# Kernel tuning notes

Hardware: AMD Instinct MI355X
Metric: run time of the kernel (lower is better)

## Reference

```python
import jax, jax.numpy as jnp
import numpy as np

N = 50000      # nodes
E = 500000     # edges (before self-loops)
IN = 128       # input feature dim
HID = 64       # hidden per head
HEADS = 8
OUT = 40       # classes
NEG_SLOPE = 0.2  # PyG GATConv default


def setup_inputs() -> dict:
    key = jax.random.key(0)
    ks = jax.random.split(key, 10)
    s = 0.05
    return {
        "x": jax.random.normal(ks[0], (N, IN), jnp.float32),
        "edge_index": jax.random.randint(ks[1], (2, E), 0, N, dtype=jnp.int32),
        "W1": jax.random.normal(ks[2], (IN, HEADS * HID), jnp.float32) * s,
        "a1_src": jax.random.normal(ks[3], (HEADS, HID), jnp.float32) * s,
        "a1_dst": jax.random.normal(ks[4], (HEADS, HID), jnp.float32) * s,
        "b1": jnp.zeros((HEADS * HID,), jnp.float32),
        "W2": jax.random.normal(ks[5], (HEADS * HID, OUT), jnp.float32) * s,
        "a2_src": jax.random.normal(ks[6], (1, OUT), jnp.float32) * s,
        "a2_dst": jax.random.normal(ks[7], (1, OUT), jnp.float32) * s,
        "b2": jnp.zeros((OUT,), jnp.float32),
    }


def gat_layer(x, src, dst, W, a_src, a_dst, b, heads, ch, concat):
    n = x.shape[0]
    h = (x @ W).reshape(n, heads, ch)                    # [N,H,C]
    e_src = jnp.einsum('nhc,hc->nh', h, a_src)           # [N,H]
    e_dst = jnp.einsum('nhc,hc->nh', h, a_dst)
    logits = jax.nn.leaky_relu(e_src[src] + e_dst[dst], NEG_SLOPE)  # [E,H]
    # segment softmax over incoming edges of each dst node
    m = jax.ops.segment_max(logits, dst, num_segments=n)
    p = jnp.exp(logits - m[dst])
    z = jax.ops.segment_sum(p, dst, num_segments=n)
    alpha = p / (z[dst] + 1e-16)                         # [E,H]
    out = jax.ops.segment_sum(h[src] * alpha[:, :, None], dst, num_segments=n)  # [N,H,C]
    out = out.reshape(n, heads * ch) if concat else out.mean(axis=1)
    return out + b


def reference(x, edge_index, W1, a1_src, a1_dst, b1, W2, a2_src, a2_dst, b2):
    loops = jnp.arange(N, dtype=edge_index.dtype)
    src = jnp.concatenate([edge_index[0], loops])        # add self-loops (PyG default)
    dst = jnp.concatenate([edge_index[1], loops])
    h = jax.nn.relu(gat_layer(x, src, dst, W1, a1_src, a1_dst, b1, HEADS, HID, True))
    h = gat_layer(h, src, dst, W2, a2_src, a2_dst, b2, 1, OUT, False)
    return jax.nn.log_softmax(h, axis=1)
```

## Files before the change

### kernel.cpp

```cpp
#include <hip/hip_runtime.h>
#include <math.h>

#define N_NODES 50000
#define E_EDGES 500000
#define E_TOT   550000
#define IN_DIM  128
#define HID     64
#define HEADS   8
#define HC      512
#define OUT_DIM 40
#define NEG_SLOPE 0.2f

__device__ __forceinline__ float leaky(float v){ return v > 0.f ? v : NEG_SLOPE * v; }


__global__ void k_hist(const int* __restrict__ ei, int* __restrict__ counts){
    int i = blockIdx.x * 256 + threadIdx.x;
    if (i < E_EDGES){
        atomicAdd(&counts[ei[E_EDGES + i]], 1);
    } else if (i < E_TOT){
        atomicAdd(&counts[i - E_EDGES], 1);
    }
}

__global__ void k_scanA(const int* __restrict__ counts, int* __restrict__ offsets,
                        int* __restrict__ blockSums){
    __shared__ int sh[1024];
    int b = blockIdx.x, t = threadIdx.x;
    int i = b * 1024 + t;
    int v = (i < N_NODES) ? counts[i] : 0;
    sh[t] = v; __syncthreads();
    for (int off = 1; off < 1024; off <<= 1){
        int add = (t >= off) ? sh[t - off] : 0;
        __syncthreads();
        sh[t] += add;
        __syncthreads();
    }
    if (i < N_NODES) offsets[i + 1] = sh[t];
    if (t == 1023) blockSums[b] = sh[t];
}

__global__ void k_scanB(int* __restrict__ blockSums, int nb){
    if (threadIdx.x == 0 && blockIdx.x == 0){
        int run = 0;
        for (int b = 0; b < nb; b++){ int v = blockSums[b]; blockSums[b] = run; run += v; }
    }
}

__global__ void k_scanC(const int* __restrict__ counts, int* __restrict__ offsets,
                        const int* __restrict__ blockSums, int* __restrict__ cursor){
    int b = blockIdx.x, t = threadIdx.x;
    int i = b * 1024 + t;
    if (i < N_NODES){
        int v = offsets[i + 1] + blockSums[b];
        offsets[i + 1] = v;
        cursor[i] = v - counts[i];
    }
    if (i == 0) offsets[0] = 0;
}

__global__ void k_scatter(const int* __restrict__ ei, int* __restrict__ cursor,
                          int* __restrict__ sortedSrc){
    int i = blockIdx.x * 256 + threadIdx.x;
    if (i < E_EDGES){
        int d = ei[E_EDGES + i];
        int pos = atomicAdd(&cursor[d], 1);
        sortedSrc[pos] = ei[i];
    } else if (i < E_TOT){
        int n = i - E_EDGES;
        int pos = atomicAdd(&cursor[n], 1);
        sortedSrc[pos] = n;
    }
}


__global__ __launch_bounds__(256) void k_gemm1e1(const float* __restrict__ x,
                                                 const float* __restrict__ W1,
                                                 const float* __restrict__ a1s,
                                                 const float* __restrict__ a1d,
                                                 float* __restrict__ h1,
                                                 float* __restrict__ e1s,
                                                 float* __restrict__ e1d){
    __shared__ float xs[16 * IN_DIM];
    const int t = threadIdx.x;
    const int row0 = blockIdx.x * 16;
    const float4* xg = (const float4*)(x + (size_t)row0 * IN_DIM);
    float4* xsv = (float4*)xs;
    xsv[t] = xg[t];
    xsv[t + 256] = xg[t + 256];
    __syncthreads();

    const int ct = t & 127;
    const int rg = t >> 7;
    float4 acc[8];
    #pragma unroll
    for (int r = 0; r < 8; r++) acc[r] = make_float4(0.f, 0.f, 0.f, 0.f);

    const float4* Wv = (const float4*)W1;
    for (int kb = 0; kb < IN_DIM; kb += 4){
        float4 w0 = Wv[(size_t)(kb + 0) * 128 + ct];
        float4 w1 = Wv[(size_t)(kb + 1) * 128 + ct];
        float4 w2 = Wv[(size_t)(kb + 2) * 128 + ct];
        float4 w3 = Wv[(size_t)(kb + 3) * 128 + ct];
        #pragma unroll
        for (int r = 0; r < 8; r++){
            float4 xv = *(const float4*)&xs[(rg * 8 + r) * IN_DIM + kb];
            acc[r].x = fmaf(xv.x, w0.x, acc[r].x); acc[r].y = fmaf(xv.x, w0.y, acc[r].y);
            acc[r].z = fmaf(xv.x, w0.z, acc[r].z); acc[r].w = fmaf(xv.x, w0.w, acc[r].w);
            acc[r].x = fmaf(xv.y, w1.x, acc[r].x); acc[r].y = fmaf(xv.y, w1.y, acc[r].y);
            acc[r].z = fmaf(xv.y, w1.z, acc[r].z); acc[r].w = fmaf(xv.y, w1.w, acc[r].w);
            acc[r].x = fmaf(xv.z, w2.x, acc[r].x); acc[r].y = fmaf(xv.z, w2.y, acc[r].y);
            acc[r].z = fmaf(xv.z, w2.z, acc[r].z); acc[r].w = fmaf(xv.z, w2.w, acc[r].w);
            acc[r].x = fmaf(xv.w, w3.x, acc[r].x); acc[r].y = fmaf(xv.w, w3.y, acc[r].y);
            acc[r].z = fmaf(xv.w, w3.z, acc[r].z); acc[r].w = fmaf(xv.w, w3.w, acc[r].w);
        }
    }

    const float4 as4 = ((const float4*)a1s)[ct];
    const float4 ad4 = ((const float4*)a1d)[ct];
    float4* h1v = (float4*)h1;
    float ps[8], pd[8];
    #pragma unroll
    for (int r = 0; r < 8; r++){
        int row = row0 + rg * 8 + r;
        h1v[(size_t)row * 128 + ct] = acc[r];
        ps[r] = acc[r].x * as4.x + acc[r].y * as4.y + acc[r].z * as4.z + acc[r].w * as4.w;
        pd[r] = acc[r].x * ad4.x + acc[r].y * ad4.y + acc[r].z * ad4.z + acc[r].w * ad4.w;
    }
    #pragma unroll
    for (int off = 1; off < 16; off <<= 1){
        #pragma unroll
        for (int r = 0; r < 8; r++){
            ps[r] += __shfl_xor(ps[r], off, 64);
            pd[r] += __shfl_xor(pd[r], off, 64);
        }
    }
    if ((t & 15) == 0){
        int h = (ct >> 4) & 7;
        #pragma unroll
        for (int r = 0; r < 8; r++){
            int row = row0 + rg * 8 + r;
            e1s[(size_t)row * HEADS + h] = ps[r];
            e1d[(size_t)row * HEADS + h] = pd[r];
        }
    }
}


__global__ __launch_bounds__(256) void k_agg1(const float* __restrict__ h1,
                                              const float* __restrict__ e1s,
                                              const float* __restrict__ e1d,
                                              const int* __restrict__ offsets,
                                              const int* __restrict__ sortedSrc,
                                              const float* __restrict__ b1,
                                              float* __restrict__ hmid){
    __shared__ int   ss[2][64];
    __shared__ float wl[2][64][8];
    __shared__ float zr[8];
    const int d = blockIdx.x;
    const int t = threadIdx.x;
    const int beg = offsets[d], end = offsets[d + 1];
    const int cnt = end - beg;
    const int nch = (cnt + 63) >> 6;
    if (t < 8) zr[t] = 0.f;

    const int jp = t & 3;
    const int el = t >> 2;
    const int hch = t >> 5;
    const float2 ed2 = *(const float2*)&e1d[(size_t)d * HEADS + 2 * jp];
    float2 zacc = make_float2(0.f, 0.f);
    float2 acc  = make_float2(0.f, 0.f);

    {
        int e = beg + el;
        if (e < end){
            int s = sortedSrc[e];
            if (jp == 0) ss[0][el] = s;
            float2 es = *(const float2*)&e1s[(size_t)s * HEADS + 2 * jp];
            float wx = __expf(leaky(es.x + ed2.x));
            float wy = __expf(leaky(es.y + ed2.y));
            *(float2*)&wl[0][el][2 * jp] = make_float2(wx, wy);
            zacc.x += wx; zacc.y += wy;
        }
    }
    __syncthreads();

    for (int c = 0; c < nch; ++c){
        int pb = c & 1;
        if (c + 1 < nch){
            int e = beg + (c + 1) * 64 + el;
            if (e < end){
                int s = sortedSrc[e];
                if (jp == 0) ss[pb ^ 1][el] = s;
                float2 es = *(const float2*)&e1s[(size_t)s * HEADS + 2 * jp];
                float wx = __expf(leaky(es.x + ed2.x));
                float wy = __expf(leaky(es.y + ed2.y));
                *(float2*)&wl[pb ^ 1][el][2 * jp] = make_float2(wx, wy);
                zacc.x += wx; zacc.y += wy;
            }
        }
        int m = cnt - c * 64; if (m > 64) m = 64;
        for (int e = 0; e < m; ++e){
            int s = ss[pb][e];
            float wv = wl[pb][e][hch];
            float2 hv = *(const float2*)&h1[(size_t)s * HC + 2 * t];
            acc.x = fmaf(wv, hv.x, acc.x);
            acc.y = fmaf(wv, hv.y, acc.y);
        }
        __syncthreads();
    }

    atomicAdd(&zr[2 * jp],     zacc.x);
    atomicAdd(&zr[2 * jp + 1], zacc.y);
    __syncthreads();
    float inv = 1.f / (zr[hch] + 1e-16f);
    float2 bv = *(const float2*)&b1[2 * t];
    float ox = fmaxf(fmaf(acc.x, inv, bv.x), 0.f);
    float oy = fmaxf(fmaf(acc.y, inv, bv.y), 0.f);
    *(float2*)&hmid[(size_t)d * HC + 2 * t] = make_float2(ox, oy);
}


__global__ __launch_bounds__(256) void k_gemm2e2(const float* __restrict__ hmid,
                                                 const float* __restrict__ W2,
                                                 const float* __restrict__ a2s,
                                                 const float* __restrict__ a2d,
                                                 float* __restrict__ h2,
                                                 float* __restrict__ e2s,
                                                 float* __restrict__ e2d){
    __shared__ float hs[64][64];
    __shared__ float ws[64 * OUT_DIM];
    const int t = threadIdx.x;
    const int row0 = blockIdx.x * 64;
    const int col = t & 63;
    const int rbase = t >> 6;
    float acc[16];
    #pragma unroll
    for (int i = 0; i < 16; i++) acc[i] = 0.f;

    for (int kb = 0; kb < HC; kb += 64){
        for (int i = t; i < 64 * 64; i += 256){
            int r = i >> 6, k = i & 63;
            int gr = row0 + r;
            hs[r][k] = (gr < N_NODES) ? hmid[(size_t)gr * HC + kb + k] : 0.f;
        }
        for (int i = t; i < 64 * OUT_DIM; i += 256){
            int k = i / OUT_DIM, j = i - k * OUT_DIM;
            ws[i] = W2[(size_t)(kb + k) * OUT_DIM + j];
        }
        __syncthreads();
        if (col < OUT_DIM){
            for (int k = 0; k < 64; k++){
                float w = ws[k * OUT_DIM + col];
                #pragma unroll
                for (int i = 0; i < 16; i++)
                    acc[i] = fmaf(hs[rbase + 4 * i][k], w, acc[i]);
            }
        }
        __syncthreads();
    }

    const float as = (col < OUT_DIM) ? a2s[col] : 0.f;
    const float ad = (col < OUT_DIM) ? a2d[col] : 0.f;
    #pragma unroll
    for (int i = 0; i < 16; i++){
        int r = row0 + rbase + 4 * i;
        bool ok = (col < OUT_DIM) && (r < N_NODES);
        float v = ok ? acc[i] : 0.f;
        if (ok) h2[(size_t)r * OUT_DIM + col] = v;
        float pvs = v * as, pvd = v * ad;
        #pragma unroll
        for (int off = 32; off > 0; off >>= 1){
            pvs += __shfl_xor(pvs, off, 64);
            pvd += __shfl_xor(pvd, off, 64);
        }
        if (col == 0 && r < N_NODES){ e2s[r] = pvs; e2d[r] = pvd; }
    }
}

__global__ __launch_bounds__(64) void k_agg2(const float* __restrict__ h2,
                                             const float* __restrict__ e2s,
                                             const float* __restrict__ e2d,
                                             const int* __restrict__ offsets,
                                             const int* __restrict__ sortedSrc,
                                             const float* __restrict__ b2,
                                             float* __restrict__ out){
    int d = blockIdx.x;
    int lane = threadIdx.x;
    int beg = offsets[d], end = offsets[d + 1];
    float ed = e2d[d];
    float acc = 0.f, z = 0.f;
    for (int e = beg; e < end; e++){
        int s = sortedSrc[e];
        float w = __expf(leaky(e2s[s] + ed));
        z += w;
        if (lane < OUT_DIM) acc = fmaf(w, h2[(size_t)s * OUT_DIM + lane], acc);
    }
    float o = acc / (z + 1e-16f) + ((lane < OUT_DIM) ? b2[lane] : 0.f);
    float ov = (lane < OUT_DIM) ? o : -INFINITY;
    float vmax = ov;
    #pragma unroll
    for (int off = 32; off > 0; off >>= 1) vmax = fmaxf(vmax, __shfl_xor(vmax, off, 64));
    float se = (lane < OUT_DIM) ? __expf(o - vmax) : 0.f;
    #pragma unroll
    for (int off = 32; off > 0; off >>= 1) se += __shfl_xor(se, off, 64);
    if (lane < OUT_DIM) out[(size_t)d * OUT_DIM + lane] = o - vmax - __logf(se);
}


extern "C" void kernel_launch(void* const* d_in, const int* in_sizes, int n_in,
                              void* d_out, int out_size, void* d_ws, size_t ws_size,
                              hipStream_t stream){
    const float* x   = (const float*)d_in[0];
    const int*   ei  = (const int*)  d_in[1];
    const float* W1  = (const float*)d_in[2];
    const float* a1s = (const float*)d_in[3];
    const float* a1d = (const float*)d_in[4];
    const float* b1  = (const float*)d_in[5];
    const float* W2  = (const float*)d_in[6];
    const float* a2s = (const float*)d_in[7];
    const float* a2d = (const float*)d_in[8];
    const float* b2  = (const float*)d_in[9];
    float* out = (float*)d_out;

    char* ws = (char*)d_ws;
    size_t off = 0;
    auto alloc = [&](size_t bytes) -> char* {
        off = (off + 255) & ~(size_t)255;
        char* p = ws + off;
        off += bytes;
        return p;
    };

    float* h1      = (float*)alloc((size_t)N_NODES * HC * 4);
    float* hmid    = (float*)alloc((size_t)N_NODES * HC * 4);
    float* h2      = (float*)alloc((size_t)N_NODES * OUT_DIM * 4);
    float* e1s     = (float*)alloc((size_t)N_NODES * HEADS * 4);
    float* e1d     = (float*)alloc((size_t)N_NODES * HEADS * 4);
    float* e2s     = (float*)alloc((size_t)N_NODES * 4);
    float* e2d     = (float*)alloc((size_t)N_NODES * 4);
    int* counts    = (int*)alloc((size_t)N_NODES * 4);
    int* offsets   = (int*)alloc((size_t)(N_NODES + 1) * 4);
    int* cursor    = (int*)alloc((size_t)N_NODES * 4);
    int* blockSums = (int*)alloc(64 * 4);
    int* sortedSrc = (int*)alloc((size_t)E_TOT * 4);

    const int nb = (N_NODES + 1023) / 1024;

    hipMemsetAsync(counts, 0, (size_t)N_NODES * 4, stream);
    k_hist   <<<(E_TOT + 255) / 256, 256, 0, stream>>>(ei, counts);
    k_scanA  <<<nb, 1024, 0, stream>>>(counts, offsets, blockSums);
    k_scanB  <<<1, 64, 0, stream>>>(blockSums, nb);
    k_scanC  <<<nb, 1024, 0, stream>>>(counts, offsets, blockSums, cursor);
    k_scatter<<<(E_TOT + 255) / 256, 256, 0, stream>>>(ei, cursor, sortedSrc);

    k_gemm1e1<<<N_NODES / 16, 256, 0, stream>>>(x, W1, a1s, a1d, h1, e1s, e1d);
    k_agg1   <<<N_NODES, 256, 0, stream>>>(h1, e1s, e1d, offsets, sortedSrc, b1, hmid);

    k_gemm2e2<<<(N_NODES + 63) / 64, 256, 0, stream>>>(hmid, W2, a2s, a2d, h2, e2s, e2d);
    k_agg2   <<<N_NODES, 64, 0, stream>>>(h2, e2s, e2d, offsets, sortedSrc, b2, out);
}
```

Before: 663.0 us.

## Map one wavefront per destination node in both aggregation kernels with register prefetch

Both aggregation kernels now assign one 64-lane wavefront to each destination node and pack four nodes per 256-thread block. Layer 1 drops the shared-memory double buffer, the block barriers and the shared atomics: each lane owns 8 channels of one head and computes that head's edge weight itself. Both kernels now load the next edge's source index and features into registers one step ahead. This removes block-level sync overhead and the idle threads in blocks that handle few edges. The cost is that the exp is recomputed in each lane, and each wave walks its edge list serially with less memory-level parallelism per node.

```diff
diff --git a/kernel.cpp b/kernel.cpp
--- a/kernel.cpp
+++ b/kernel.cpp
@@ -154,70 +154,58 @@
                                               const int* __restrict__ sortedSrc,
                                               const float* __restrict__ b1,
                                               float* __restrict__ hmid){
-    __shared__ int   ss[2][64];
-    __shared__ float wl[2][64][8];
-    __shared__ float zr[8];
-    const int d = blockIdx.x;
-    const int t = threadIdx.x;
+    const int lane = threadIdx.x & 63;
+    const int d = blockIdx.x * 4 + (threadIdx.x >> 6);
+    if (d >= N_NODES) return;
     const int beg = offsets[d], end = offsets[d + 1];
     const int cnt = end - beg;
-    const int nch = (cnt + 63) >> 6;
-    if (t < 8) zr[t] = 0.f;
-
-    const int jp = t & 3;
-    const int el = t >> 2;
-    const int hch = t >> 5;
-    const float2 ed2 = *(const float2*)&e1d[(size_t)d * HEADS + 2 * jp];
-    float2 zacc = make_float2(0.f, 0.f);
-    float2 acc  = make_float2(0.f, 0.f);
-
+    const int h = lane >> 3;
+    const int c0 = lane * 8;
+    const float ed = e1d[(size_t)d * HEADS + h];
+
+    float4 acc0 = make_float4(0.f,0.f,0.f,0.f), acc1 = make_float4(0.f,0.f,0.f,0.f);
+    float z = 0.f;
+
+    int s1 = 0, s2 = 0;
+    float eA = 0.f; float4 hA0, hA1;
     {
-        int e = beg + el;
-        if (e < end){
-            int s = sortedSrc[e];
-            if (jp == 0) ss[0][el] = s;
-            float2 es = *(const float2*)&e1s[(size_t)s * HEADS + 2 * jp];
-            float wx = __expf(leaky(es.x + ed2.x));
-            float wy = __expf(leaky(es.y + ed2.y));
-            *(float2*)&wl[0][el][2 * jp] = make_float2(wx, wy);
-            zacc.x += wx; zacc.y += wy;
-        }
-    }
-    __syncthreads();
-
-    for (int c = 0; c < nch; ++c){
-        int pb = c & 1;
-        if (c + 1 < nch){
-            int e = beg + (c + 1) * 64 + el;
-            if (e < end){
-                int s = sortedSrc[e];
-                if (jp == 0) ss[pb ^ 1][el] = s;
-                float2 es = *(const float2*)&e1s[(size_t)s * HEADS + 2 * jp];
-                float wx = __expf(leaky(es.x + ed2.x));
-                float wy = __expf(leaky(es.y + ed2.y));
-                *(float2*)&wl[pb ^ 1][el][2 * jp] = make_float2(wx, wy);
-                zacc.x += wx; zacc.y += wy;
-            }
-        }
-        int m = cnt - c * 64; if (m > 64) m = 64;
-        for (int e = 0; e < m; ++e){
-            int s = ss[pb][e];
-            float wv = wl[pb][e][hch];
-            float2 hv = *(const float2*)&h1[(size_t)s * HC + 2 * t];
-            acc.x = fmaf(wv, hv.x, acc.x);
-            acc.y = fmaf(wv, hv.y, acc.y);
-        }
-        __syncthreads();
-    }
-
-    atomicAdd(&zr[2 * jp],     zacc.x);
-    atomicAdd(&zr[2 * jp + 1], zacc.y);
-    __syncthreads();
-    float inv = 1.f / (zr[hch] + 1e-16f);
-    float2 bv = *(const float2*)&b1[2 * t];
-    float ox = fmaxf(fmaf(acc.x, inv, bv.x), 0.f);
-    float oy = fmaxf(fmaf(acc.y, inv, bv.y), 0.f);
-    *(float2*)&hmid[(size_t)d * HC + 2 * t] = make_float2(ox, oy);
+        int s0 = sortedSrc[beg];
+        eA = e1s[(size_t)s0 * HEADS + h];
+        const float4* hp = (const float4*)(h1 + (size_t)s0 * HC + c0);
+        hA0 = hp[0]; hA1 = hp[1];
+        if (cnt > 1) s1 = sortedSrc[beg + 1];
+    }
+    for (int e = 0; e < cnt; ++e){
+        if (e + 2 < cnt) s2 = sortedSrc[beg + e + 2];
+        float eB = 0.f; float4 hB0, hB1;
+        if (e + 1 < cnt){
+            eB = e1s[(size_t)s1 * HEADS + h];
+            const float4* hp = (const float4*)(h1 + (size_t)s1 * HC + c0);
+            hB0 = hp[0]; hB1 = hp[1];
+        }
+        float w = __expf(leaky(eA + ed));
+        z += w;
+        acc0.x = fmaf(w, hA0.x, acc0.x); acc0.y = fmaf(w, hA0.y, acc0.y);
+        acc0.z = fmaf(w, hA0.z, acc0.z); acc0.w = fmaf(w, hA0.w, acc0.w);
+        acc1.x = fmaf(w, hA1.x, acc1.x); acc1.y = fmaf(w, hA1.y, acc1.y);
+        acc1.z = fmaf(w, hA1.z, acc1.z); acc1.w = fmaf(w, hA1.w, acc1.w);
+        eA = eB; hA0 = hB0; hA1 = hB1; s1 = s2;
+    }
+
+    const float inv = 1.f / (z + 1e-16f);
+    const float4 bv0 = ((const float4*)b1)[lane * 2];
+    const float4 bv1 = ((const float4*)b1)[lane * 2 + 1];
+    float4 o0, o1;
+    o0.x = fmaxf(fmaf(acc0.x, inv, bv0.x), 0.f);
+    o0.y = fmaxf(fmaf(acc0.y, inv, bv0.y), 0.f);
+    o0.z = fmaxf(fmaf(acc0.z, inv, bv0.z), 0.f);
+    o0.w = fmaxf(fmaf(acc0.w, inv, bv0.w), 0.f);
+    o1.x = fmaxf(fmaf(acc1.x, inv, bv1.x), 0.f);
+    o1.y = fmaxf(fmaf(acc1.y, inv, bv1.y), 0.f);
+    o1.z = fmaxf(fmaf(acc1.z, inv, bv1.z), 0.f);
+    o1.w = fmaxf(fmaf(acc1.w, inv, bv1.w), 0.f);
+    float4* op = (float4*)(hmid + (size_t)d * HC + c0);
+    op[0] = o0; op[1] = o1;
 }
 
 
@@ -278,33 +266,53 @@
     }
 }
 
-__global__ __launch_bounds__(64) void k_agg2(const float* __restrict__ h2,
-                                             const float* __restrict__ e2s,
-                                             const float* __restrict__ e2d,
-                                             const int* __restrict__ offsets,
-                                             const int* __restrict__ sortedSrc,
-                                             const float* __restrict__ b2,
-                                             float* __restrict__ out){
-    int d = blockIdx.x;
-    int lane = threadIdx.x;
-    int beg = offsets[d], end = offsets[d + 1];
-    float ed = e2d[d];
+
+__global__ __launch_bounds__(256) void k_agg2(const float* __restrict__ h2,
+                                              const float* __restrict__ e2s,
+                                              const float* __restrict__ e2d,
+                                              const int* __restrict__ offsets,
+                                              const int* __restrict__ sortedSrc,
+                                              const float* __restrict__ b2,
+                                              float* __restrict__ out){
+    const int lane = threadIdx.x & 63;
+    const int d = blockIdx.x * 4 + (threadIdx.x >> 6);
+    if (d >= N_NODES) return;
+    const int beg = offsets[d], end = offsets[d + 1];
+    const int cnt = end - beg;
+    const float ed = e2d[d];
+    const bool act = (lane < OUT_DIM);
+
     float acc = 0.f, z = 0.f;
-    for (int e = beg; e < end; e++){
-        int s = sortedSrc[e];
-        float w = __expf(leaky(e2s[s] + ed));
+    int s1 = 0, s2 = 0;
+    float eA = 0.f, hA = 0.f;
+    {
+        int s0 = sortedSrc[beg];
+        eA = e2s[s0];
+        if (act) hA = h2[(size_t)s0 * OUT_DIM + lane];
+        if (cnt > 1) s1 = sortedSrc[beg + 1];
+    }
+    for (int e = 0; e < cnt; ++e){
+        if (e + 2 < cnt) s2 = sortedSrc[beg + e + 2];
+        float eB = 0.f, hB = 0.f;
+        if (e + 1 < cnt){
+            eB = e2s[s1];
+            if (act) hB = h2[(size_t)s1 * OUT_DIM + lane];
+        }
+        float w = __expf(leaky(eA + ed));
         z += w;
-        if (lane < OUT_DIM) acc = fmaf(w, h2[(size_t)s * OUT_DIM + lane], acc);
-    }
-    float o = acc / (z + 1e-16f) + ((lane < OUT_DIM) ? b2[lane] : 0.f);
-    float ov = (lane < OUT_DIM) ? o : -INFINITY;
+        acc = fmaf(w, hA, acc);
+        eA = eB; hA = hB; s1 = s2;
+    }
+
+    float o = acc / (z + 1e-16f) + (act ? b2[lane] : 0.f);
+    float ov = act ? o : -INFINITY;
     float vmax = ov;
     #pragma unroll
     for (int off = 32; off > 0; off >>= 1) vmax = fmaxf(vmax, __shfl_xor(vmax, off, 64));
-    float se = (lane < OUT_DIM) ? __expf(o - vmax) : 0.f;
+    float se = act ? __expf(o - vmax) : 0.f;
     #pragma unroll
     for (int off = 32; off > 0; off >>= 1) se += __shfl_xor(se, off, 64);
-    if (lane < OUT_DIM) out[(size_t)d * OUT_DIM + lane] = o - vmax - __logf(se);
+    if (act) out[(size_t)d * OUT_DIM + lane] = o - vmax - __logf(se);
 }
 
 
@@ -355,8 +363,8 @@
     k_scatter<<<(E_TOT + 255) / 256, 256, 0, stream>>>(ei, cursor, sortedSrc);
 
     k_gemm1e1<<<N_NODES / 16, 256, 0, stream>>>(x, W1, a1s, a1d, h1, e1s, e1d);
-    k_agg1   <<<N_NODES, 256, 0, stream>>>(h1, e1s, e1d, offsets, sortedSrc, b1, hmid);
+    k_agg1   <<<(N_NODES + 3) / 4, 256, 0, stream>>>(h1, e1s, e1d, offsets, sortedSrc, b1, hmid);
 
     k_gemm2e2<<<(N_NODES + 63) / 64, 256, 0, stream>>>(hmid, W2, a2s, a2d, h2, e2s, e2d);
-    k_agg2   <<<N_NODES, 64, 0, stream>>>(h2, e2s, e2d, offsets, sortedSrc, b2, out);
-}
+    k_agg2   <<<(N_NODES + 3) / 4, 256, 0, stream>>>(h2, e2s, e2d, offsets, sortedSrc, b2, out);
+}
```

Measured after the change: 644.1 us. -2.9%, faster.
